# Kernel optimization log

Measured on AMD Instinct MI355X. Metric: run time of the kernel, lower is better.

## Reference

```python
import jax, jax.numpy as jnp
import numpy as np

NB_STEPS = 50  # Clenshaw-Curtis quadrature with NB_STEPS+1 points
B = 16384


def _cc_weights(nb_steps):
    # Faithful port of UMNN compute_cc_weights (ParallelNeuralIntegral)
    lam = np.arange(nb_steps + 1, dtype=np.float64).reshape(-1, 1)
    lam = np.cos((lam @ lam.T) * np.pi / nb_steps)
    lam[:, 0] *= 0.5
    lam[:, -1] *= 0.5
    lam = lam * 2.0 / nb_steps
    k = np.arange(nb_steps + 1, dtype=np.float64).reshape(-1, 1)
    den = 1.0 - k ** 2
    den[0] = 1.0
    den[np.arange(1, nb_steps + 1, 2)] = 1.0  # avoid div-by-zero; zeroed below
    W = 2.0 / den
    W[0] = 1.0
    W[np.arange(1, nb_steps + 1, 2)] = 0.0
    cc_w = (lam.T @ W).astype(np.float32)  # [S, 1]
    steps = np.cos(np.arange(nb_steps + 1).reshape(-1, 1) * np.pi / nb_steps).astype(np.float32)  # [S, 1]
    return jnp.asarray(cc_w), jnp.asarray(steps)


def _integrand(xh, w1, b1, w2, b2, w3, b3, w4, b4):
    # IntegrandNN: Linear+ReLU x3, Linear+ELU, then +1 (guarantees positivity-ish)
    a = jax.nn.relu(xh @ w1 + b1)
    a = jax.nn.relu(a @ w2 + b2)
    a = jax.nn.relu(a @ w3 + b3)
    a = jax.nn.elu(a @ w4 + b4)
    return a + 1.0


def setup_inputs() -> dict:
    key = jax.random.key(0)
    ks = jax.random.split(key, 10)
    s = 0.1  # small weight scale for numerical sanity
    return {
        "x": jax.random.normal(ks[0], (B, 1), dtype=jnp.float32),
        "h": jax.random.normal(ks[1], (B, 1), dtype=jnp.float32),
        "w1": jax.random.normal(ks[2], (2, 128), dtype=jnp.float32) * s,
        "b1": jax.random.normal(ks[3], (128,), dtype=jnp.float32) * s,
        "w2": jax.random.normal(ks[4], (128, 128), dtype=jnp.float32) * s,
        "b2": jax.random.normal(ks[5], (128,), dtype=jnp.float32) * s,
        "w3": jax.random.normal(ks[6], (128, 128), dtype=jnp.float32) * s,
        "b3": jax.random.normal(ks[7], (128,), dtype=jnp.float32) * s,
        "w4": jax.random.normal(ks[8], (128, 1), dtype=jnp.float32) * s,
        "b4": jax.random.normal(ks[9], (1,), dtype=jnp.float32) * s,
    }


def reference(x, h, w1, b1, w2, b2, w3, b3, w4, b4):
    cc_w, steps = _cc_weights(NB_STEPS)  # [S,1], [S,1]
    S = NB_STEPS + 1
    x0 = jnp.zeros_like(x)
    xT = x  # x0 + nb_steps * (x - x0) / nb_steps
    # quadrature abscissae mapped to [x0, xT]: [B, S, 1]
    X = x0[:, None, :] + (xT - x0)[:, None, :] * (steps[None, :, :] + 1.0) * 0.5
    hh = jnp.broadcast_to(h[:, None, :], (x.shape[0], S, h.shape[1]))
    xh = jnp.concatenate([X, hh], axis=-1).reshape(x.shape[0] * S, -1)  # [B*S, in_d]
    dz = _integrand(xh, w1, b1, w2, b2, w3, b3, w4, b4).reshape(x.shape[0], S, -1)
    z = jnp.sum(dz * cc_w[None, :, :], axis=1) * (xT - x0) * 0.5  # [B, out_d]
    # MonotonicNN.forward: integral + offset (offset = h); self.net(h) output is discarded
    return z + h
```

## Files before the change

### kernel.cpp

```cpp
#include <hip/hip_runtime.h>
#include <hip/hip_bf16.h>

#define NSTEP 50
#define S51 51
#define HID 128
#define MT 64
#define BPB 16
#define RPB (BPB * S51)
#define NTILE 13
#define GRID (16384 / BPB)
#define BLOCK 256

typedef __attribute__((ext_vector_type(4))) float floatx4;
typedef __attribute__((ext_vector_type(16))) float floatx16;
typedef __attribute__((ext_vector_type(8))) __bf16 bf16x8;

__device__ __forceinline__ unsigned pk4_fp8(float v0, float v1, float v2, float v3) {
    unsigned r = (unsigned)__builtin_amdgcn_cvt_pk_fp8_f32(v0, v1, 0, false);
    r = (unsigned)__builtin_amdgcn_cvt_pk_fp8_f32(v2, v3, (int)r, true);
    return r;
}


__device__ __forceinline__ floatx16 ld_bias16(const float* bs, int base) {
    const floatx4 t0 = *(const floatx4*)(&bs[base]);
    const floatx4 t1 = *(const floatx4*)(&bs[base + 8]);
    const floatx4 t2 = *(const floatx4*)(&bs[base + 16]);
    const floatx4 t3 = *(const floatx4*)(&bs[base + 24]);
    floatx16 v = {t0[0], t0[1], t0[2], t0[3], t1[0], t1[1], t1[2], t1[3],
                  t2[0], t2[1], t2[2], t2[3], t3[0], t3[1], t3[2], t3[3]};
    return v;
}

__device__ __forceinline__ void l1_tile(unsigned char* dst, int t,
                                        const float* tsp,
                                        bf16x8 aw, float xv, __bf16 hb, float hm,
                                        int wbm, int l31, int hi, int mi) {
    const int s1 = 4 * t + (l31 >> 4);
    bf16x8 bx0 = {}, bx1 = {};
    bx0[0] = (__bf16)(xv * tsp[s1] * hm);     bx0[1] = hb;  bx0[2] = (__bf16)hm;
    bx1[0] = (__bf16)(xv * tsp[s1 + 2] * hm); bx1[1] = hb;  bx1[2] = (__bf16)hm;
    const floatx16 zz = {};
    floatx16 d0 = __builtin_amdgcn_mfma_f32_32x32x16_bf16(aw, bx0, zz, 0, 0, 0);
    floatx16 d1 = __builtin_amdgcn_mfma_f32_32x32x16_bf16(aw, bx1, zz, 0, 0, 0);
#pragma unroll
    for (int g = 0; g < 4; ++g) {
        unsigned p0 = pk4_fp8(fmaxf(d0[4 * g + 0], 0.0f), fmaxf(d0[4 * g + 1], 0.0f),
                              fmaxf(d0[4 * g + 2], 0.0f), fmaxf(d0[4 * g + 3], 0.0f));
        *(unsigned*)(&dst[wbm ^ (g << 3)]) = p0;
        unsigned p1 = pk4_fp8(fmaxf(d1[4 * g + 0], 0.0f), fmaxf(d1[4 * g + 1], 0.0f),
                              fmaxf(d1[4 * g + 2], 0.0f), fmaxf(d1[4 * g + 3], 0.0f));
        *(unsigned*)(&dst[(wbm ^ (g << 3)) + 4096]) = p1;
    }
}

template<int PA, bool CONS, bool L2P, bool L3P, bool L1P>
__device__ __forceinline__ void phase(int s,
        unsigned char (&A1)[2][MT * HID], unsigned char (&A2)[2][MT * HID],
        float (&posum)[2][4][MT],
        const float* b2s, const float* b3s, const float* w4s,
        const float* fs, const float* ts,
        float& accq, const long (&w2f)[8], const long (&w3f)[8],
        bf16x8 aw, float xv, __bf16 hb, float hm, float b4v,
        int rbh, int wbm, int tid, int l31, int hi, int mi) {
    constexpr int PB = PA ^ 1;
    if (CONS) {
        if (tid < MT) {
            int lr = (s - 2) * MT + tid;
            float u = posum[PA][0][tid] + posum[PA][1][tid] + posum[PA][2][tid]
                    + posum[PA][3][tid] + b4v;
            float dz = u > 0.0f ? u + 1.0f : __expf(u);
            accq += dz * fs[lr >> 4];
        }
    }
    if (L2P) {
        const floatx16 ci = ld_bias16(b2s, mi * 32 + 4 * hi);
        long f0 = *(const long*)(&A1[PA][rbh]);
        long f1 = *(const long*)(&A1[PA][rbh + 4096]);
        floatx16 a0 = __builtin_amdgcn_mfma_f32_32x32x16_fp8_fp8(w2f[0], f0, ci, 0, 0, 0);
        floatx16 a1 = __builtin_amdgcn_mfma_f32_32x32x16_fp8_fp8(w2f[0], f1, ci, 0, 0, 0);
#pragma unroll
        for (int kc = 1; kc < 8; ++kc) {
            f0 = *(const long*)(&A1[PA][rbh ^ (kc << 4)]);
            f1 = *(const long*)(&A1[PA][(rbh ^ (kc << 4)) + 4096]);
            a0 = __builtin_amdgcn_mfma_f32_32x32x16_fp8_fp8(w2f[kc], f0, a0, 0, 0, 0);
            a1 = __builtin_amdgcn_mfma_f32_32x32x16_fp8_fp8(w2f[kc], f1, a1, 0, 0, 0);
        }
#pragma unroll
        for (int g = 0; g < 4; ++g) {
            unsigned p0 = pk4_fp8(fmaxf(a0[4 * g + 0], 0.0f), fmaxf(a0[4 * g + 1], 0.0f),
                                  fmaxf(a0[4 * g + 2], 0.0f), fmaxf(a0[4 * g + 3], 0.0f));
            *(unsigned*)(&A2[PA][wbm ^ (g << 3)]) = p0;
            unsigned p1 = pk4_fp8(fmaxf(a1[4 * g + 0], 0.0f), fmaxf(a1[4 * g + 1], 0.0f),
                                  fmaxf(a1[4 * g + 2], 0.0f), fmaxf(a1[4 * g + 3], 0.0f));
            *(unsigned*)(&A2[PA][(wbm ^ (g << 3)) + 4096]) = p1;
        }
    }
    if (L3P) {
        const floatx16 ci = ld_bias16(b3s, mi * 32 + 4 * hi);
        long g0 = *(const long*)(&A2[PB][rbh]);
        long g1 = *(const long*)(&A2[PB][rbh + 4096]);
        floatx16 c0 = __builtin_amdgcn_mfma_f32_32x32x16_fp8_fp8(w3f[0], g0, ci, 0, 0, 0);
        floatx16 c1 = __builtin_amdgcn_mfma_f32_32x32x16_fp8_fp8(w3f[0], g1, ci, 0, 0, 0);
#pragma unroll
        for (int kc = 1; kc < 8; ++kc) {
            g0 = *(const long*)(&A2[PB][rbh ^ (kc << 4)]);
            g1 = *(const long*)(&A2[PB][(rbh ^ (kc << 4)) + 4096]);
            c0 = __builtin_amdgcn_mfma_f32_32x32x16_fp8_fp8(w3f[kc], g0, c0, 0, 0, 0);
            c1 = __builtin_amdgcn_mfma_f32_32x32x16_fp8_fp8(w3f[kc], g1, c1, 0, 0, 0);
        }
        float p0 = 0.0f, p1 = 0.0f;
#pragma unroll
        for (int g = 0; g < 4; ++g) {
            const floatx4 w4v = *(const floatx4*)(&w4s[mi * 32 + 8 * g + 4 * hi]);
#pragma unroll
            for (int rr = 0; rr < 4; ++rr) {
                p0 = fmaf(fmaxf(c0[4 * g + rr], 0.0f), w4v[rr], p0);
                p1 = fmaf(fmaxf(c1[4 * g + rr], 0.0f), w4v[rr], p1);
            }
        }
        p0 += __shfl_xor(p0, 32);
        p1 += __shfl_xor(p1, 32);
        if (hi == 0) {
            posum[PB][mi][l31] = p0;
            posum[PB][mi][l31 + 32] = p1;
        }
    }
    if (L1P) {
        l1_tile(A1[PB], s + 1, ts, aw, xv, hb, hm, wbm, l31, hi, mi);
    }
    __syncthreads();
}

__launch_bounds__(BLOCK, 4)
__global__ void monotonic_fused(const float* __restrict__ x, const float* __restrict__ h,
                                const float* __restrict__ w1, const float* __restrict__ b1,
                                const float* __restrict__ w2, const float* __restrict__ b2,
                                const float* __restrict__ w3, const float* __restrict__ b3,
                                const float* __restrict__ w4, const float* __restrict__ b4,
                                float* __restrict__ out) {
    __shared__ __align__(16) unsigned char A1[2][MT * HID];
    __shared__ __align__(16) unsigned char A2[2][MT * HID];
    __shared__ float b2s[HID], b3s[HID], w4s[HID];
    __shared__ float fs[S51], ts[56];
    __shared__ float xs[BPB], hs[BPB];
    __shared__ float posum[2][4][MT];

    const int tid = threadIdx.x;
    const int lane = tid & 63;
    const int mi = tid >> 6;
    const int l31 = lane & 31;
    const int hi = lane >> 5;

    if (tid < HID) {
        b2s[tid] = b2[tid]; b3s[tid] = b3[tid]; w4s[tid] = w4[tid];
    }
    if (tid < BPB) {
        xs[tid] = x[blockIdx.x * BPB + tid];
        hs[tid] = h[blockIdx.x * BPB + tid];
    }
    if (tid < 56) {
        if (tid < S51) {
            const float PI50 = 0.06283185307179586f;
            float acc = 1.0f;
            for (int i = 2; i <= 50; i += 2) {
                int m = (i * tid) % 100;
                acc += (2.0f / (1.0f - (float)(i * i))) * cosf((float)m * PI50);
            }
            float ccw = acc * 0.04f * ((tid == 0 || tid == NSTEP) ? 0.5f : 1.0f);
            fs[tid] = ccw * 0.5f;
            ts[tid] = (cosf((float)tid * PI50) + 1.0f) * 0.5f;
        } else {
            ts[tid] = 0.0f;
        }
    }
    const float b4v = b4[0];
    const float hm = (hi == 0) ? 1.0f : 0.0f;

    long w2f[8], w3f[8];
    {
        const int irow = mi * 32 + l31;
#pragma unroll
        for (int kc = 0; kc < 8; ++kc) {
            const int kb = kc * 16 + hi * 8;
            unsigned lo2 = pk4_fp8(w2[(kb + 0) * HID + irow], w2[(kb + 1) * HID + irow],
                                   w2[(kb + 2) * HID + irow], w2[(kb + 3) * HID + irow]);
            unsigned hi2 = pk4_fp8(w2[(kb + 4) * HID + irow], w2[(kb + 5) * HID + irow],
                                   w2[(kb + 6) * HID + irow], w2[(kb + 7) * HID + irow]);
            w2f[kc] = (long)(((unsigned long long)hi2 << 32) | lo2);
            unsigned lo3 = pk4_fp8(w3[(kb + 0) * HID + irow], w3[(kb + 1) * HID + irow],
                                   w3[(kb + 2) * HID + irow], w3[(kb + 3) * HID + irow]);
            unsigned hi3 = pk4_fp8(w3[(kb + 4) * HID + irow], w3[(kb + 5) * HID + irow],
                                   w3[(kb + 6) * HID + irow], w3[(kb + 7) * HID + irow]);
            w3f[kc] = (long)(((unsigned long long)hi3 << 32) | lo3);
        }
    }
    bf16x8 aw = {};
    {
        const int j = mi * 32 + l31;
        aw[0] = (__bf16)(w1[j] * hm);
        aw[1] = (__bf16)(w1[HID + j] * hm);
        aw[2] = (__bf16)(b1[j] * hm);
    }
    __syncthreads();

    const float xv = xs[l31 & 15];
    const __bf16 hb = (__bf16)(hs[l31 & 15] * hm);
    float accq = 0.0f;

    const int rb  = l31 * HID + ((l31 & 15) << 3);
    const int rbh = rb ^ (hi << 3);
    const int wbm = (rb + 4 * hi) ^ (mi << 5);

    l1_tile(A1[0], 0, ts, aw, xv, hb, hm, wbm, l31, hi, mi);
    __syncthreads();

#define PHASE_ARGS A1, A2, posum, b2s, b3s, w4s, fs, ts, accq, w2f, w3f, \
                   aw, xv, hb, hm, b4v, rbh, wbm, tid, l31, hi, mi
    phase<0, false, true, false, true >(0, PHASE_ARGS);
    phase<1, false, true, true,  true >(1, PHASE_ARGS);
    for (int it = 0; it < 5; ++it) {
        phase<0, true, true, true, true>(2 + 2 * it, PHASE_ARGS);
        phase<1, true, true, true, true>(3 + 2 * it, PHASE_ARGS);
    }
    phase<0, true, true,  true, true >(12, PHASE_ARGS);
    phase<1, true, false, true, false>(13, PHASE_ARGS);
#undef PHASE_ARGS

    if (tid < MT) {
        int lr = (NTILE - 1) * MT + tid;
        if (lr < RPB) {
            float u = posum[0][0][tid] + posum[0][1][tid] + posum[0][2][tid]
                    + posum[0][3][tid] + b4v;
            float dz = u > 0.0f ? u + 1.0f : __expf(u);
            accq += dz * fs[lr >> 4];
        }
        accq += __shfl_xor(accq, 16);
        accq += __shfl_xor(accq, 32);
        if (tid < BPB) out[blockIdx.x * BPB + tid] = hs[tid] + accq * xs[tid];
    }
}

extern "C" void kernel_launch(void* const* d_in, const int* in_sizes, int n_in,
                              void* d_out, int out_size, void* d_ws, size_t ws_size,
                              hipStream_t stream) {
    const float* x  = (const float*)d_in[0];
    const float* h  = (const float*)d_in[1];
    const float* w1 = (const float*)d_in[2];
    const float* b1 = (const float*)d_in[3];
    const float* w2 = (const float*)d_in[4];
    const float* b2 = (const float*)d_in[5];
    const float* w3 = (const float*)d_in[6];
    const float* b3 = (const float*)d_in[7];
    const float* w4 = (const float*)d_in[8];
    const float* b4 = (const float*)d_in[9];
    float* out = (float*)d_out;

    monotonic_fused<<<GRID, BLOCK, 0, stream>>>(x, h, w1, b1, w2, b2, w3, b3, w4, b4, out);
}
```

Before: 129.1 us.

## Fuse layer-1 into layer-2 via register operands, dropping A1 LDS buffer

Result: slower. 158.3 us (+22.6%).

```diff
diff --git a/kernel.cpp b/kernel.cpp
--- a/kernel.cpp
+++ b/kernel.cpp
@@ -32,36 +32,22 @@
     return v;
 }
 
-__device__ __forceinline__ void l1_tile(unsigned char* dst, int t,
-                                        const float* tsp,
-                                        bf16x8 aw, float xv, __bf16 hb, float hm,
-                                        int wbm, int l31, int hi, int mi) {
-    const int s1 = 4 * t + (l31 >> 4);
-    bf16x8 bx0 = {}, bx1 = {};
-    bx0[0] = (__bf16)(xv * tsp[s1] * hm);     bx0[1] = hb;  bx0[2] = (__bf16)hm;
-    bx1[0] = (__bf16)(xv * tsp[s1 + 2] * hm); bx1[1] = hb;  bx1[2] = (__bf16)hm;
-    const floatx16 zz = {};
-    floatx16 d0 = __builtin_amdgcn_mfma_f32_32x32x16_bf16(aw, bx0, zz, 0, 0, 0);
-    floatx16 d1 = __builtin_amdgcn_mfma_f32_32x32x16_bf16(aw, bx1, zz, 0, 0, 0);
+__device__ __forceinline__ void pack_row(unsigned char* dst, floatx16 a, int wb) {
 #pragma unroll
     for (int g = 0; g < 4; ++g) {
-        unsigned p0 = pk4_fp8(fmaxf(d0[4 * g + 0], 0.0f), fmaxf(d0[4 * g + 1], 0.0f),
-                              fmaxf(d0[4 * g + 2], 0.0f), fmaxf(d0[4 * g + 3], 0.0f));
-        *(unsigned*)(&dst[wbm ^ (g << 3)]) = p0;
-        unsigned p1 = pk4_fp8(fmaxf(d1[4 * g + 0], 0.0f), fmaxf(d1[4 * g + 1], 0.0f),
-                              fmaxf(d1[4 * g + 2], 0.0f), fmaxf(d1[4 * g + 3], 0.0f));
-        *(unsigned*)(&dst[(wbm ^ (g << 3)) + 4096]) = p1;
-    }
-}
-
-template<int PA, bool CONS, bool L2P, bool L3P, bool L1P>
+        unsigned p = pk4_fp8(fmaxf(a[4 * g + 0], 0.0f), fmaxf(a[4 * g + 1], 0.0f),
+                             fmaxf(a[4 * g + 2], 0.0f), fmaxf(a[4 * g + 3], 0.0f));
+        *(unsigned*)(&dst[wb ^ (g << 3)]) = p;
+    }
+}
+
+template<int PA, bool CONS, bool L2P, bool L3P>
 __device__ __forceinline__ void phase(int s,
-        unsigned char (&A1)[2][MT * HID], unsigned char (&A2)[2][MT * HID],
-        float (&posum)[2][4][MT],
+        unsigned char (&A2)[2][MT * HID], float (&posum)[2][4][MT],
         const float* b2s, const float* b3s, const float* w4s,
         const float* fs, const float* ts,
         float& accq, const long (&w2f)[8], const long (&w3f)[8],
-        bf16x8 aw, float xv, __bf16 hb, float hm, float b4v,
+        const bf16x8 (&aw)[4], float xv, __bf16 hb, float hm, float b4v,
         int rbh, int wbm, int tid, int l31, int hi, int mi) {
     constexpr int PB = PA ^ 1;
     if (CONS) {
@@ -73,29 +59,6 @@
             accq += dz * fs[lr >> 4];
         }
     }
-    if (L2P) {
-        const floatx16 ci = ld_bias16(b2s, mi * 32 + 4 * hi);
-        long f0 = *(const long*)(&A1[PA][rbh]);
-        long f1 = *(const long*)(&A1[PA][rbh + 4096]);
-        floatx16 a0 = __builtin_amdgcn_mfma_f32_32x32x16_fp8_fp8(w2f[0], f0, ci, 0, 0, 0);
-        floatx16 a1 = __builtin_amdgcn_mfma_f32_32x32x16_fp8_fp8(w2f[0], f1, ci, 0, 0, 0);
-#pragma unroll
-        for (int kc = 1; kc < 8; ++kc) {
-            f0 = *(const long*)(&A1[PA][rbh ^ (kc << 4)]);
-            f1 = *(const long*)(&A1[PA][(rbh ^ (kc << 4)) + 4096]);
-            a0 = __builtin_amdgcn_mfma_f32_32x32x16_fp8_fp8(w2f[kc], f0, a0, 0, 0, 0);
-            a1 = __builtin_amdgcn_mfma_f32_32x32x16_fp8_fp8(w2f[kc], f1, a1, 0, 0, 0);
-        }
-#pragma unroll
-        for (int g = 0; g < 4; ++g) {
-            unsigned p0 = pk4_fp8(fmaxf(a0[4 * g + 0], 0.0f), fmaxf(a0[4 * g + 1], 0.0f),
-                                  fmaxf(a0[4 * g + 2], 0.0f), fmaxf(a0[4 * g + 3], 0.0f));
-            *(unsigned*)(&A2[PA][wbm ^ (g << 3)]) = p0;
-            unsigned p1 = pk4_fp8(fmaxf(a1[4 * g + 0], 0.0f), fmaxf(a1[4 * g + 1], 0.0f),
-                                  fmaxf(a1[4 * g + 2], 0.0f), fmaxf(a1[4 * g + 3], 0.0f));
-            *(unsigned*)(&A2[PA][(wbm ^ (g << 3)) + 4096]) = p1;
-        }
-    }
     if (L3P) {
         const floatx16 ci = ld_bias16(b3s, mi * 32 + 4 * hi);
         long g0 = *(const long*)(&A2[PB][rbh]);
@@ -126,8 +89,36 @@
             posum[PB][mi][l31 + 32] = p1;
         }
     }
-    if (L1P) {
-        l1_tile(A1[PB], s + 1, ts, aw, xv, hb, hm, wbm, l31, hi, mi);
+    if (L2P) {
+        const floatx16 ci = ld_bias16(b2s, mi * 32 + 4 * hi);
+        const int s1 = 4 * s + (l31 >> 4);
+        const floatx16 zz = {};
+#pragma unroll
+        for (int rg = 0; rg < 2; ++rg) {
+            bf16x8 bx = {};
+            bx[0] = (__bf16)(xv * ts[s1 + 2 * rg] * hm);
+            bx[1] = hb;  bx[2] = (__bf16)hm;
+            long bf[8];
+#pragma unroll
+            for (int q = 0; q < 4; ++q) {
+                floatx16 d = __builtin_amdgcn_mfma_f32_32x32x16_bf16(aw[q], bx, zz, 0, 0, 0);
+                unsigned u0 = pk4_fp8(fmaxf(d[0], 0.0f), fmaxf(d[1], 0.0f),
+                                      fmaxf(d[2], 0.0f), fmaxf(d[3], 0.0f));
+                unsigned u1 = pk4_fp8(fmaxf(d[4], 0.0f), fmaxf(d[5], 0.0f),
+                                      fmaxf(d[6], 0.0f), fmaxf(d[7], 0.0f));
+                unsigned u2 = pk4_fp8(fmaxf(d[8], 0.0f), fmaxf(d[9], 0.0f),
+                                      fmaxf(d[10], 0.0f), fmaxf(d[11], 0.0f));
+                unsigned u3 = pk4_fp8(fmaxf(d[12], 0.0f), fmaxf(d[13], 0.0f),
+                                      fmaxf(d[14], 0.0f), fmaxf(d[15], 0.0f));
+                bf[2 * q]     = (long)(((unsigned long long)u1 << 32) | u0);
+                bf[2 * q + 1] = (long)(((unsigned long long)u3 << 32) | u2);
+            }
+            floatx16 a = __builtin_amdgcn_mfma_f32_32x32x16_fp8_fp8(w2f[0], bf[0], ci, 0, 0, 0);
+#pragma unroll
+            for (int kc = 1; kc < 8; ++kc)
+                a = __builtin_amdgcn_mfma_f32_32x32x16_fp8_fp8(w2f[kc], bf[kc], a, 0, 0, 0);
+            pack_row(&A2[PA][4096 * rg], a, wbm);
+        }
     }
     __syncthreads();
 }
@@ -139,7 +130,6 @@
                                 const float* __restrict__ w3, const float* __restrict__ b3,
                                 const float* __restrict__ w4, const float* __restrict__ b4,
                                 float* __restrict__ out) {
-    __shared__ __align__(16) unsigned char A1[2][MT * HID];
     __shared__ __align__(16) unsigned char A2[2][MT * HID];
     __shared__ float b2s[HID], b3s[HID], w4s[HID];
     __shared__ float fs[S51], ts[56];
@@ -182,12 +172,13 @@
         const int irow = mi * 32 + l31;
 #pragma unroll
         for (int kc = 0; kc < 8; ++kc) {
+            const int pb = (kc >> 1) * 32 + (kc & 1) * 16 + 4 * hi;
+            unsigned lo2 = pk4_fp8(w2[(pb + 0) * HID + irow], w2[(pb + 1) * HID + irow],
+                                   w2[(pb + 2) * HID + irow], w2[(pb + 3) * HID + irow]);
+            unsigned hi2 = pk4_fp8(w2[(pb + 8) * HID + irow], w2[(pb + 9) * HID + irow],
+                                   w2[(pb + 10) * HID + irow], w2[(pb + 11) * HID + irow]);
+            w2f[kc] = (long)(((unsigned long long)hi2 << 32) | lo2);
             const int kb = kc * 16 + hi * 8;
-            unsigned lo2 = pk4_fp8(w2[(kb + 0) * HID + irow], w2[(kb + 1) * HID + irow],
-                                   w2[(kb + 2) * HID + irow], w2[(kb + 3) * HID + irow]);
-            unsigned hi2 = pk4_fp8(w2[(kb + 4) * HID + irow], w2[(kb + 5) * HID + irow],
-                                   w2[(kb + 6) * HID + irow], w2[(kb + 7) * HID + irow]);
-            w2f[kc] = (long)(((unsigned long long)hi2 << 32) | lo2);
             unsigned lo3 = pk4_fp8(w3[(kb + 0) * HID + irow], w3[(kb + 1) * HID + irow],
                                    w3[(kb + 2) * HID + irow], w3[(kb + 3) * HID + irow]);
             unsigned hi3 = pk4_fp8(w3[(kb + 4) * HID + irow], w3[(kb + 5) * HID + irow],
@@ -195,12 +186,15 @@
             w3f[kc] = (long)(((unsigned long long)hi3 << 32) | lo3);
         }
     }
-    bf16x8 aw = {};
-    {
-        const int j = mi * 32 + l31;
-        aw[0] = (__bf16)(w1[j] * hm);
-        aw[1] = (__bf16)(w1[HID + j] * hm);
-        aw[2] = (__bf16)(b1[j] * hm);
+    bf16x8 aw[4];
+#pragma unroll
+    for (int q = 0; q < 4; ++q) {
+        const int j = q * 32 + l31;
+        bf16x8 t = {};
+        t[0] = (__bf16)(w1[j] * hm);
+        t[1] = (__bf16)(w1[HID + j] * hm);
+        t[2] = (__bf16)(b1[j] * hm);
+        aw[q] = t;
     }
     __syncthreads();
 
@@ -212,28 +206,24 @@
     const int rbh = rb ^ (hi << 3);
     const int wbm = (rb + 4 * hi) ^ (mi << 5);
 
-    l1_tile(A1[0], 0, ts, aw, xv, hb, hm, wbm, l31, hi, mi);
-    __syncthreads();
-
-#define PHASE_ARGS A1, A2, posum, b2s, b3s, w4s, fs, ts, accq, w2f, w3f, \
+#define PHASE_ARGS A2, posum, b2s, b3s, w4s, fs, ts, accq, w2f, w3f, \
                    aw, xv, hb, hm, b4v, rbh, wbm, tid, l31, hi, mi
-    phase<0, false, true, false, true >(0, PHASE_ARGS);
-    phase<1, false, true, true,  true >(1, PHASE_ARGS);
+    phase<0, false, true,  false>(0, PHASE_ARGS);
+    phase<1, false, true,  true >(1, PHASE_ARGS);
     for (int it = 0; it < 5; ++it) {
-        phase<0, true, true, true, true>(2 + 2 * it, PHASE_ARGS);
-        phase<1, true, true, true, true>(3 + 2 * it, PHASE_ARGS);
-    }
-    phase<0, true, true,  true, true >(12, PHASE_ARGS);
-    phase<1, true, false, true, false>(13, PHASE_ARGS);
+        phase<0, true, true, true>(2 + 2 * it, PHASE_ARGS);
+        phase<1, true, true, true>(3 + 2 * it, PHASE_ARGS);
+    }
+    phase<0, true, true,  true>(12, PHASE_ARGS);
+    phase<1, true, false, true>(13, PHASE_ARGS);
 #undef PHASE_ARGS
 
     if (tid < MT) {
-        int lr = (NTILE - 1) * MT + tid;
-        if (lr < RPB) {
+        if (tid < RPB - (NTILE - 1) * MT) {
             float u = posum[0][0][tid] + posum[0][1][tid] + posum[0][2][tid]
                     + posum[0][3][tid] + b4v;
             float dz = u > 0.0f ? u + 1.0f : __expf(u);
-            accq += dz * fs[lr >> 4];
+            accq += dz * fs[((NTILE - 1) * MT + tid) >> 4];
         }
         accq += __shfl_xor(accq, 16);
         accq += __shfl_xor(accq, 32);
```
